# Performance work log

Measured on AMD Instinct MI355X. Metric: run time of the kernel, lower is better.

Reference implementation:

```python
import jax, jax.numpy as jnp
import numpy as np

LOG2PI = 1.837877  # exact constant used in source zeta()
K = 4              # pruning width (init arg k)


def _trans_child_multi(S00, S01, S11, tm0, tm1, g_mu, g_var):
    """Multiply 2D transition gaussian N([xc,xp]; t_mu, Sigma) with 1D child
    gaussian N(xc; g_mu, g_var), integrate out xc.
    Returns (log_scale, mu, var) of the resulting gaussian over the parent xp.
    Uses explicit 2x2 inverse/determinant exactly as the torch source does."""
    det_S = S00 * S11 - S01 * S01
    inv_det = 1.0 / det_S
    l00 = S11 * inv_det      # Lambda1 = Sigma^-1 (symmetric 2x2)
    l01 = -S01 * inv_det
    l11 = S00 * inv_det
    e1_0 = l00 * tm0 + l01 * tm1   # eta1 = Lambda1 @ t_mu
    e1_1 = l01 * tm0 + l11 * tm1
    # zeta1 = -0.5*(2*log2pi - log|Lambda1| + eta1^T Sigma eta1); log|Lambda1| = -log det_S
    q1 = e1_0 * (S00 * e1_0 + S01 * e1_1) + e1_1 * (S01 * e1_0 + S11 * e1_1)
    zeta1 = -0.5 * (2.0 * LOG2PI + jnp.log(det_S) + q1)
    lam2 = 1.0 / g_var
    zeta2 = -0.5 * (LOG2PI + jnp.log(g_var) + g_mu * g_mu * lam2)
    # Lambda_multi = Lambda1 + [[lam2,0],[0,0]]
    lm00 = l00 + lam2
    det_m = lm00 * l11 - l01 * l01
    inv_m = 1.0 / det_m
    vm00 = l11 * inv_m       # V_multi = Lambda_multi^-1
    vm01 = -l01 * inv_m
    vm11 = lm00 * inv_m
    em0 = e1_0 + g_mu * lam2  # eta_multi = eta1 + [eta2, 0]
    em1 = e1_1
    qm = em0 * (vm00 * em0 + vm01 * em1) + em1 * (vm01 * em0 + vm11 * em1)
    zetam = -0.5 * (2.0 * LOG2PI - jnp.log(det_m) + qm)
    scale = zeta1 + zeta2 - zetam
    mu = vm01 * em0 + vm11 * em1   # marginal over parent dim (second block)
    var = vm11
    return scale, mu, var


def _gauss1d_multi(m1, v1, m2, v2):
    """Product of two 1D gaussians -> (log_scale, mu, var)."""
    lam = 1.0 / v1 + 1.0 / v2
    vm = 1.0 / lam
    em = m1 / v1 + m2 / v2
    z1 = -0.5 * (LOG2PI + jnp.log(v1) + m1 * m1 / v1)
    z2 = -0.5 * (LOG2PI + jnp.log(v2) + m2 * m2 / v2)
    zm = -0.5 * (LOG2PI + jnp.log(vm) + em * em * vm)
    return z1 + z2 - zm, vm * em, vm


def setup_inputs():
    key = jax.random.key(0)
    k0, k1, k2, k3, k4, k5, k6 = jax.random.split(key, 7)
    B, L, V, NL = 64, 512, 150000, 46   # NL = num_labels(45) + 1 pad label
    tokens = jax.random.randint(k0, (B, L), 0, V)
    s_weight_table = 0.1 * jax.random.normal(k1, (V, NL), jnp.float32)
    s_mu_table = jax.random.normal(k2, (V, NL), jnp.float32)
    # var embeddings squared (A A^T for 1x1) in forward; keep away from 0
    s_var_table = 1.0 + 0.1 * jax.random.normal(k3, (V, NL), jnp.float32)
    t_weight = 0.1 * jax.random.normal(k4, (NL, NL), jnp.float32)
    t_mu = jax.random.normal(k5, (NL, NL, 2), jnp.float32)
    t_var_p = 1.0 + 0.1 * jax.random.normal(k6, (NL, NL, 3), jnp.float32)
    return {"tokens": tokens, "s_weight_table": s_weight_table,
            "s_mu_table": s_mu_table, "s_var_table": s_var_table,
            "t_weight": t_weight, "t_mu": t_mu, "t_var_p": t_var_p}


def _forward(tokens, s_weight_table, s_mu_table, s_var_table, t_weight, t_mu, t_var_p):
    B, L = tokens.shape
    NL = t_weight.shape[0]
    # state (emission) gaussian params via embedding lookups
    s_w = s_weight_table[tokens]            # [B,L,NL]
    s_m = s_mu_table[tokens]                # [B,L,NL]
    s_v = jnp.square(s_var_table[tokens])   # A A^T for the 1x1 case  [B,L,NL]
    # transition covariance: A = [[v0, v1], [0, v2]], Sigma = A A^T (as in source)
    v0, v1, v2 = t_var_p[..., 0], t_var_p[..., 1], t_var_p[..., 2]
    S00 = v0 * v0 + v1 * v1                 # [NL,NL]
    S01 = v1 * v2
    S11 = v2 * v2
    tm0, tm1 = t_mu[..., 0], t_mu[..., 1]
    NEG = jnp.float32(-1e30)

    def step(carry, xs):
        sc, mu, va = carry                  # inside mixture [B,K,NL] over child labels
        sw_t, sm_t, sv_t = xs               # emission at the next position [B,NL]
        scale2, mu2, var2 = _trans_child_multi(
            S00, S01, S11, tm0, tm1, mu[..., None], va[..., None])  # [B,K,C,P]
        scale2 = scale2 + sc[..., None] + t_weight
        # pruning: merge (component, child-label) dims, top-k per parent label
        def flat(x):
            return x.transpose(0, 3, 1, 2).reshape(B, NL, -1)   # [B,P,K*C]
        fs = flat(scale2)
        top_s, top_i = jax.lax.top_k(fs, K)                     # [B,P,K]
        top_m = jnp.take_along_axis(flat(mu2), top_i, axis=-1)
        top_v = jnp.take_along_axis(flat(var2), top_i, axis=-1)
        top_s = top_s.transpose(0, 2, 1)                        # [B,K,P]
        top_m = top_m.transpose(0, 2, 1)
        top_v = top_v.transpose(0, 2, 1)
        # multiply emission gaussian at the new position
        es, em, ev = _gauss1d_multi(top_m, top_v, sm_t[:, None, :], sv_t[:, None, :])
        new_sc = top_s + es + sw_t[:, None, :]
        return (new_sc, em, ev), None

    # init: emission at position 0 as the single real component, padded to K
    pad = jnp.full((B, K - 1, NL), NEG)
    sc0 = jnp.concatenate([s_w[:, 0][:, None], pad], axis=1)
    mu0 = jnp.concatenate([s_m[:, 0][:, None], jnp.zeros((B, K - 1, NL))], axis=1)
    va0 = jnp.concatenate([s_v[:, 0][:, None], jnp.ones((B, K - 1, NL))], axis=1)
    xs = (jnp.swapaxes(s_w[:, 1:], 0, 1),
          jnp.swapaxes(s_m[:, 1:], 0, 1),
          jnp.swapaxes(s_v[:, 1:], 0, 1))
    (sc, mu, va), _ = jax.lax.scan(step, (sc0, mu0, va0), xs)
    # each final gaussian integrates to exp(scale); inside score = logsumexp
    return jax.scipy.special.logsumexp(sc.reshape(B, -1), axis=-1)   # [B]


def reference(tokens, s_weight_table, s_mu_table, s_var_table, t_weight, t_mu, t_var_p):
    return _forward(tokens, s_weight_table, s_mu_table, s_var_table,
                    t_weight, t_mu, t_var_p)
```

## Files before the change

### kernel.cpp

```cpp
#include <hip/hip_runtime.h>

#define LOG2PI 1.837877f
#define LN2 0.6931471805599453f
#define RLN2 1.4426950408889634f
#define NLAB 46
#define KK 4
#define LSEQ 512
#define KC 184
#define BLOCK 832
#define NA 736
#define EMB 768

__device__ __forceinline__ float fastrcp(float x){ return __builtin_amdgcn_rcpf(x); }
__device__ __forceinline__ float flog2(float x){ return __builtin_amdgcn_logf(x); }
__device__ __forceinline__ float fmed3(float a, float b, float c){
    return __builtin_amdgcn_fmed3f(a, b, c);
}
template<int CTRL>
__device__ __forceinline__ float dppq(float v){
    return __uint_as_float((unsigned)__builtin_amdgcn_mov_dpp(
        (int)__float_as_uint(v), CTRL, 0xF, 0xF, false));
}
template<int OFF>
__device__ __forceinline__ float swz(float v){
    return __uint_as_float((unsigned)__builtin_amdgcn_ds_swizzle(
        (int)__float_as_uint(v), OFF));
}
template<int N> struct IC { static constexpr int value = N; };

__global__ __launch_bounds__(BLOCK, 4) void lveg_kernel(
    const int* __restrict__ tokens,
    const float* __restrict__ s_w_tab,
    const float* __restrict__ s_m_tab,
    const float* __restrict__ s_v_tab,
    const float* __restrict__ t_weight,
    const float* __restrict__ t_mu,
    const float* __restrict__ t_var_p,
    float* __restrict__ out)
{
    __shared__ float4 lam2v[2][NLAB];
    __shared__ float4 glamv[2][NLAB];
    __shared__ float4 z2sv[2][NLAB];
    __shared__ float  scv[KC];
    __shared__ float4 emi[2][NLAB];
    __shared__ int    tokL[LSEQ];
    __shared__ float4 tabA[NLAB*NLAB];
    __shared__ float2 tabB[NLAB*NLAB];

    const int b = blockIdx.x;
    const int tid = threadIdx.x;
    const int s = tid & 15;
    const int p = tid >> 4;
    const bool isA = (p < NLAB);
    const unsigned vmask2 = (s < 14) ? 0xFFFFFFFFu : 0u;
    const unsigned vorm2  = (s < 14) ? 0u : 0xFF800000u;
    const int c2 = (s < 14) ? (s + 32) : 0;
    const float NEGINF = __uint_as_float(0xFF800000u);

    for (int cp = tid; cp < NLAB*NLAB; cp += BLOCK) {
        float v0 = t_var_p[cp*3+0], v1 = t_var_p[cp*3+1], v2 = t_var_p[cp*3+2];
        float tm0 = t_mu[cp*2+0],  tm1 = t_mu[cp*2+1];
        float S00 = v0*v0 + v1*v1, S01 = v1*v2, S11 = v2*v2;
        float det = S00*S11 - S01*S01;
        float inv = 1.0f / det;
        float l00 = S11*inv, l01 = -S01*inv, l11 = S00*inv;
        float e0 = l00*tm0 + l01*tm1;
        float e1 = l01*tm0 + l11*tm1;
        float q1 = e0*(S00*e0 + S01*e1) + e1*(S01*e0 + S11*e1);
        float zeta1 = -0.5f*(2.0f*LOG2PI + __logf(det) + q1);
        tabA[cp] = make_float4(e0, e1, inv, l11);
        tabB[cp] = make_float2(l01, zeta1 + LOG2PI + t_weight[cp]);
    }
    for (int i = tid; i < LSEQ; i += BLOCK) tokL[i] = tokens[b*LSEQ + i];

    float rce0[3], rl11[3], rinv[3], rl11s[3], rqbs[3], rqes[3], rqcs[3], rAs[3];
    if (isA) {
#pragma unroll
        for (int ci = 0; ci < 3; ++ci) {
            int c = s + 16*ci;
            if (c < NLAB) {
                int cp = c*NLAB + p;
                float v0 = t_var_p[cp*3+0], v1 = t_var_p[cp*3+1], v2 = t_var_p[cp*3+2];
                float tm0 = t_mu[cp*2+0],  tm1 = t_mu[cp*2+1];
                float S00 = v0*v0 + v1*v1, S01 = v1*v2, S11 = v2*v2;
                float det = S00*S11 - S01*S01;
                float inv = 1.0f / det;
                float l00 = S11*inv, l01 = -S01*inv, l11 = S00*inv;
                float e0 = l00*tm0 + l01*tm1;
                float e1 = l01*tm0 + l11*tm1;
                float q1 = e0*(S00*e0 + S01*e1) + e1*(S01*e0 + S11*e1);
                float zeta1 = -0.5f*(2.0f*LOG2PI + __logf(det) + q1);
                rce0[ci]  = e0;
                rl11[ci]  = l11;
                rinv[ci]  = inv;
                rl11s[ci] = l11 * RLN2;
                rqbs[ci]  = 2.0f*l01*e1 * RLN2;
                rqes[ci]  = e1*e1 * RLN2;
                rqcs[ci]  = l00*e1*e1 * RLN2;
                rAs[ci]   = (zeta1 + LOG2PI + t_weight[cp]) * RLN2;
            } else {
                rce0[ci]=0.f; rl11[ci]=0.f; rinv[ci]=1.f; rl11s[ci]=0.f;
                rqbs[ci]=0.f; rqes[ci]=0.f; rqcs[ci]=0.f; rAs[ci]=0.f;
            }
        }
    }

    if (tid < NLAB) {
        int tok0 = tokens[b * LSEQ];
        float sw  = s_w_tab[tok0*NLAB + tid];
        float sm  = s_m_tab[tok0*NLAB + tid];
        float svr = s_v_tab[tok0*NLAB + tid];
        float gv = svr*svr;
        float lam2 = 1.0f / gv;
        float glam = sm * lam2;
        float z2 = -0.5f*(LOG2PI + __logf(gv) + sm*glam);
        float zpad = (-1e30f - 0.5f*LOG2PI) * RLN2;
        lam2v[0][tid] = make_float4(lam2, 1.0f, 1.0f, 1.0f);
        glamv[0][tid] = make_float4(glam, 0.0f, 0.0f, 0.0f);
        z2sv[0][tid]  = make_float4((sw + z2) * RLN2, zpad, zpad, zpad);
    }
    if (tid >= EMB) {
        int pe = tid - EMB;
        if (pe < NLAB) {
            int tok = tokens[b*LSEQ + 1];
            float sw  = s_w_tab[tok*NLAB + pe];
            float sm  = s_m_tab[tok*NLAB + pe];
            float svr = s_v_tab[tok*NLAB + pe];
            float sv = svr*svr;
            float rs = 1.0f / sv;
            float eb = sm * rs;
            float ez = -0.5f*(LOG2PI + __logf(sv) + sm*eb);
            emi[1][pe] = make_float4(sw, rs, eb, ez);
        }
    }
    __syncthreads();

    auto stepf = [&](auto CC, int t) {
        constexpr int CUR = decltype(CC)::value;
        if (isA) {
            float4 L0 = lam2v[CUR][s],      G0 = glamv[CUR][s],      Z0 = z2sv[CUR][s];
            float4 L1 = lam2v[CUR][s + 16], G1 = glamv[CUR][s + 16], Z1 = z2sv[CUR][s + 16];
            float4 L2 = lam2v[CUR][c2],     G2 = glamv[CUR][c2],     Z2 = z2sv[CUR][c2];
            __builtin_amdgcn_sched_barrier(0);
            float t0=NEGINF, t1=NEGINF, t2=NEGINF, t3=NEGINF;
#define CAND(ci, k, lam2, glam, z2s) {                                        \
            float em0 = rce0[ci] + (glam);                                    \
            float dm  = fmaf((lam2), rl11[ci], rinv[ci]);                     \
            float tA  = fmaf(rl11s[ci], em0, -rqbs[ci]);                      \
            float tB  = fmaf((lam2), rqes[ci], rqcs[ci]);                     \
            float Q   = fmaf(em0, tA, tB);                                    \
            float key = fmaf(0.5f, fmaf(Q, fastrcp(dm), -flog2(dm)),          \
                             rAs[ci] + (z2s));                                \
            unsigned kb = (__float_as_uint(key) & 0xFFFFFF00u)                \
                        | (unsigned)((k)*NLAB + s + 16*(ci));                 \
            if ((ci) == 2) kb = (kb & vmask2) | vorm2;                        \
            float fk = __uint_as_float(kb);                                   \
            float n0 = fmaxf(t0, fk);                                         \
            float n1 = fmed3(fk, t0, t1);                                     \
            float n2 = fmed3(fk, t1, t2);                                     \
            float n3 = fmed3(fk, t2, t3);                                     \
            t0=n0; t1=n1; t2=n2; t3=n3; }
            CAND(0, 0, L0.x, G0.x, Z0.x)  CAND(0, 1, L0.y, G0.y, Z0.y)
            CAND(0, 2, L0.z, G0.z, Z0.z)  CAND(0, 3, L0.w, G0.w, Z0.w)
            CAND(1, 0, L1.x, G1.x, Z1.x)  CAND(1, 1, L1.y, G1.y, Z1.y)
            CAND(1, 2, L1.z, G1.z, Z1.z)  CAND(1, 3, L1.w, G1.w, Z1.w)
            CAND(2, 0, L2.x, G2.x, Z2.x)  CAND(2, 1, L2.y, G2.y, Z2.y)
            CAND(2, 2, L2.z, G2.z, Z2.z)  CAND(2, 3, L2.w, G2.w, Z2.w)
#undef CAND
#define MSTAGE(F) { float b0=F(t0), b1=F(t1), b2=F(t2), b3=F(t3);                 \
                float M0=fmaxf(t0,b3), M1=fmaxf(t1,b2), M2=fmaxf(t2,b1), M3=fmaxf(t3,b0); \
                float x;                                                          \
                x=fmaxf(M0,M2); M2=fminf(M0,M2); M0=x;  x=fmaxf(M1,M3); M3=fminf(M1,M3); M1=x; \
                x=fmaxf(M0,M1); M1=fminf(M0,M1); M0=x;  x=fmaxf(M2,M3); M3=fminf(M2,M3); M2=x; \
                t0=M0; t1=M1; t2=M2; t3=M3; }
            MSTAGE(dppq<0xB1>)
            MSTAGE(dppq<0x4E>)
            MSTAGE(swz<0x101F>)
            {
                float b0=swz<0x201F>(t0), b1=swz<0x201F>(t1),
                      b2=swz<0x201F>(t2), b3=swz<0x201F>(t3);
                float M0=fmaxf(t0,b3), M1=fmaxf(t1,b2), M2=fmaxf(t2,b1), M3=fmaxf(t3,b0);
                t0=M0; t1=M1; t2=M2; t3=M3;
            }
#undef MSTAGE
            if (s < 4) {
                float sel = (s==0)?t0 : (s==1)?t1 : (s==2)?t2 : t3;
                unsigned kc = __float_as_uint(sel) & 0xFFu;
                unsigned k  = (kc * 1428u) >> 16;
                int c  = (int)kc - (int)k*NLAB;
                int cp = c*NLAB + p;
                float4 ta = tabA[cp];
                float2 tb = tabB[cp];
                float lam2 = ((const float*)&lam2v[CUR][0])[4*c + (int)k];
                float glam = ((const float*)&glamv[CUR][0])[4*c + (int)k];
                float z2s  = ((const float*)&z2sv[CUR][0])[4*c + (int)k] * LN2;
                float em0 = ta.x + glam;
                float em1 = ta.y;
                float l01 = tb.x;
                float l00 = fmaf(l01, l01, ta.z) * fastrcp(ta.w);
                float dm  = fmaf(lam2, ta.w, ta.z);
                float rdm = fastrcp(dm);
                float lm00 = l00 + lam2;
                float Q = fmaf(em0, fmaf(ta.w, em0, -2.0f*l01*em1), lm00*em1*em1);
                float score = fmaf(0.5f, fmaf(Q, rdm, -__logf(dm)), tb.y + z2s);
                float mu2  = rdm*(lm00*em1 - l01*em0);
                float var2 = lm00*rdm;
                float4 ev = emi[CUR ^ 1][p];
                float rv1 = fastrcp(var2);
                float lam = rv1 + ev.y;
                float emm = fmaf(mu2, rv1, ev.z);
                float vm  = fastrcp(lam);
                float z1 = -0.5f*(LOG2PI + __logf(var2) + mu2*mu2*rv1);
                float zm = -0.5f*(LOG2PI + __logf(vm) + emm*emm*vm);
                float nsc = score + (z1 + ev.w - zm) + ev.x;
                ((float*)&lam2v[CUR^1][p])[s] = lam;
                ((float*)&glamv[CUR^1][p])[s] = emm;
                ((float*)&z2sv[CUR^1][p])[s]  = (nsc + zm) * RLN2;
                scv[(int)s*NLAB + p] = nsc;
            }
        } else if (tid >= EMB) {
            int pe = tid - EMB;
            if (pe < NLAB && t + 1 < LSEQ) {
                int tok = tokL[t + 1];
                float sw  = s_w_tab[tok*NLAB + pe];
                float sm  = s_m_tab[tok*NLAB + pe];
                float svr = s_v_tab[tok*NLAB + pe];
                float sv = svr*svr;
                float rs = 1.0f / sv;
                float eb = sm * rs;
                float ez = -0.5f*(LOG2PI + __logf(sv) + sm*eb);
                emi[CUR][pe] = make_float4(sw, rs, eb, ez);
            }
        }
        __syncthreads();
    };

    int t = 1;
#pragma unroll 1
    for (int it = 0; it < (LSEQ - 2) / 2; ++it) {
        stepf(IC<0>{}, t); ++t;
        stepf(IC<1>{}, t); ++t;
    }
    stepf(IC<0>{}, t);

    if (tid < 64) {
        float mx = -1e38f;
        for (int i = tid; i < KC; i += 64) mx = fmaxf(mx, scv[i]);
#pragma unroll
        for (int m = 32; m; m >>= 1) mx = fmaxf(mx, __shfl_xor(mx, m, 64));
        float sum = 0.0f;
        for (int i = tid; i < KC; i += 64) sum += __expf(scv[i] - mx);
#pragma unroll
        for (int m = 32; m; m >>= 1) sum += __shfl_xor(sum, m, 64);
        if (tid == 0) out[b] = mx + __logf(sum);
    }
}

extern "C" void kernel_launch(void* const* d_in, const int* in_sizes, int n_in,
                              void* d_out, int out_size, void* d_ws, size_t ws_size,
                              hipStream_t stream) {
    const int*   tokens = (const int*)d_in[0];
    const float* sw     = (const float*)d_in[1];
    const float* sm     = (const float*)d_in[2];
    const float* sv     = (const float*)d_in[3];
    const float* tw     = (const float*)d_in[4];
    const float* tmu    = (const float*)d_in[5];
    const float* tvp    = (const float*)d_in[6];
    float* o = (float*)d_out;
    hipLaunchKernelGGL(lveg_kernel, dim3(64), dim3(BLOCK), 0, stream,
                       tokens, sw, sm, sv, tw, tmu, tvp, o);
}
```

Measured before the change: 1.182 ms.

## Pack per-component state into float2 pairs and vectorize candidate scoring

Replaces the three separate float4 shared arrays (lam2, glam, z2s) with one interleaved array of float2 pairs per label, grouped by pairs of pruned components. The candidate key computation is rewritten on 2-wide vectors so the compiler can emit packed FP32 operations (v_pk_fma/v_pk_mul) for two components at once. The goal is fewer VALU instructions in the hot per-step scoring loop. It adds strided index math for reads and writes, and the LDS load pattern changes from float4 to 64-bit loads, which may change bank behaviour.

```diff
diff --git a/kernel.cpp b/kernel.cpp
--- a/kernel.cpp
+++ b/kernel.cpp
@@ -11,6 +11,8 @@
 #define NA 736
 #define EMB 768
 
+typedef float v2f __attribute__((ext_vector_type(2)));
+
 __device__ __forceinline__ float fastrcp(float x){ return __builtin_amdgcn_rcpf(x); }
 __device__ __forceinline__ float flog2(float x){ return __builtin_amdgcn_logf(x); }
 __device__ __forceinline__ float fmed3(float a, float b, float c){
@@ -38,10 +40,8 @@
     const float* __restrict__ t_var_p,
     float* __restrict__ out)
 {
-    __shared__ float4 lam2v[2][NLAB];
-    __shared__ float4 glamv[2][NLAB];
-    __shared__ float4 z2sv[2][NLAB];
-    __shared__ float  scv[KC];
+    __shared__ v2f   pkc[2][NLAB][6];
+    __shared__ float scv[KC];
     __shared__ float4 emi[2][NLAB];
     __shared__ int    tokL[LSEQ];
     __shared__ float4 tabA[NLAB*NLAB];
@@ -115,9 +115,13 @@
         float glam = sm * lam2;
         float z2 = -0.5f*(LOG2PI + __logf(gv) + sm*glam);
         float zpad = (-1e30f - 0.5f*LOG2PI) * RLN2;
-        lam2v[0][tid] = make_float4(lam2, 1.0f, 1.0f, 1.0f);
-        glamv[0][tid] = make_float4(glam, 0.0f, 0.0f, 0.0f);
-        z2sv[0][tid]  = make_float4((sw + z2) * RLN2, zpad, zpad, zpad);
+        v2f r;
+        r.x = lam2; r.y = 1.0f;            pkc[0][tid][0] = r;
+        r.x = glam; r.y = 0.0f;            pkc[0][tid][1] = r;
+        r.x = (sw + z2)*RLN2; r.y = zpad;  pkc[0][tid][2] = r;
+        r.x = 1.0f; r.y = 1.0f;            pkc[0][tid][3] = r;
+        r.x = 0.0f; r.y = 0.0f;            pkc[0][tid][4] = r;
+        r.x = zpad; r.y = zpad;            pkc[0][tid][5] = r;
     }
     if (tid >= EMB) {
         int pe = tid - EMB;
@@ -138,21 +142,17 @@
     auto stepf = [&](auto CC, int t) {
         constexpr int CUR = decltype(CC)::value;
         if (isA) {
-            float4 L0 = lam2v[CUR][s],      G0 = glamv[CUR][s],      Z0 = z2sv[CUR][s];
-            float4 L1 = lam2v[CUR][s + 16], G1 = glamv[CUR][s + 16], Z1 = z2sv[CUR][s + 16];
-            float4 L2 = lam2v[CUR][c2],     G2 = glamv[CUR][c2],     Z2 = z2sv[CUR][c2];
+            const int cc[3] = {s, s + 16, c2};
+            v2f q[3][6];
+#pragma unroll
+            for (int ci = 0; ci < 3; ++ci)
+#pragma unroll
+                for (int j = 0; j < 6; ++j)
+                    q[ci][j] = pkc[CUR][cc[ci]][j];
             __builtin_amdgcn_sched_barrier(0);
             float t0=NEGINF, t1=NEGINF, t2=NEGINF, t3=NEGINF;
-#define CAND(ci, k, lam2, glam, z2s) {                                        \
-            float em0 = rce0[ci] + (glam);                                    \
-            float dm  = fmaf((lam2), rl11[ci], rinv[ci]);                     \
-            float tA  = fmaf(rl11s[ci], em0, -rqbs[ci]);                      \
-            float tB  = fmaf((lam2), rqes[ci], rqcs[ci]);                     \
-            float Q   = fmaf(em0, tA, tB);                                    \
-            float key = fmaf(0.5f, fmaf(Q, fastrcp(dm), -flog2(dm)),          \
-                             rAs[ci] + (z2s));                                \
-            unsigned kb = (__float_as_uint(key) & 0xFFFFFF00u)                \
-                        | (unsigned)((k)*NLAB + s + 16*(ci));                 \
+#define INS(kf, id, ci) {                                                     \
+            unsigned kb = (__float_as_uint(kf) & 0xFFFFFF00u) | (unsigned)(id); \
             if ((ci) == 2) kb = (kb & vmask2) | vorm2;                        \
             float fk = __uint_as_float(kb);                                   \
             float n0 = fmaxf(t0, fk);                                         \
@@ -160,13 +160,27 @@
             float n2 = fmed3(fk, t1, t2);                                     \
             float n3 = fmed3(fk, t2, t3);                                     \
             t0=n0; t1=n1; t2=n2; t3=n3; }
-            CAND(0, 0, L0.x, G0.x, Z0.x)  CAND(0, 1, L0.y, G0.y, Z0.y)
-            CAND(0, 2, L0.z, G0.z, Z0.z)  CAND(0, 3, L0.w, G0.w, Z0.w)
-            CAND(1, 0, L1.x, G1.x, Z1.x)  CAND(1, 1, L1.y, G1.y, Z1.y)
-            CAND(1, 2, L1.z, G1.z, Z1.z)  CAND(1, 3, L1.w, G1.w, Z1.w)
-            CAND(2, 0, L2.x, G2.x, Z2.x)  CAND(2, 1, L2.y, G2.y, Z2.y)
-            CAND(2, 2, L2.z, G2.z, Z2.z)  CAND(2, 3, L2.w, G2.w, Z2.w)
-#undef CAND
+#define CANDP(ci, pr) {                                                       \
+            v2f lamP  = q[ci][3*(pr)+0];                                      \
+            v2f glamP = q[ci][3*(pr)+1];                                      \
+            v2f zP    = q[ci][3*(pr)+2];                                      \
+            v2f em0 = glamP + rce0[ci];                                       \
+            v2f dm  = lamP * rl11[ci] + rinv[ci];                             \
+            v2f tA  = em0 * rl11s[ci] - rqbs[ci];                             \
+            v2f tB  = lamP * rqes[ci] + rqcs[ci];                             \
+            v2f Q   = em0 * tA + tB;                                          \
+            v2f rdm; rdm.x = fastrcp(dm.x); rdm.y = fastrcp(dm.y);            \
+            v2f lg;  lg.x  = flog2(dm.x);   lg.y  = flog2(dm.y);              \
+            v2f base  = zP + rAs[ci];                                         \
+            v2f inner = Q * rdm - lg;                                         \
+            v2f keyP  = 0.5f * inner + base;                                  \
+            INS(keyP.x, (2*(pr))*NLAB   + s + 16*(ci), ci)                    \
+            INS(keyP.y, (2*(pr)+1)*NLAB + s + 16*(ci), ci) }
+            CANDP(0, 0) CANDP(0, 1)
+            CANDP(1, 0) CANDP(1, 1)
+            CANDP(2, 0) CANDP(2, 1)
+#undef CANDP
+#undef INS
 #define MSTAGE(F) { float b0=F(t0), b1=F(t1), b2=F(t2), b3=F(t3);                 \
                 float M0=fmaxf(t0,b3), M1=fmaxf(t1,b2), M2=fmaxf(t2,b1), M3=fmaxf(t3,b0); \
                 float x;                                                          \
@@ -191,9 +205,11 @@
                 int cp = c*NLAB + p;
                 float4 ta = tabA[cp];
                 float2 tb = tabB[cp];
-                float lam2 = ((const float*)&lam2v[CUR][0])[4*c + (int)k];
-                float glam = ((const float*)&glamv[CUR][0])[4*c + (int)k];
-                float z2s  = ((const float*)&z2sv[CUR][0])[4*c + (int)k] * LN2;
+                const float* sp = (const float*)&pkc[CUR][c][0]
+                                  + 6*(int)(k >> 1) + (int)(k & 1);
+                float lam2 = sp[0];
+                float glam = sp[2];
+                float z2s  = sp[4] * LN2;
                 float em0 = ta.x + glam;
                 float em1 = ta.y;
                 float l01 = tb.x;
@@ -213,10 +229,11 @@
                 float z1 = -0.5f*(LOG2PI + __logf(var2) + mu2*mu2*rv1);
                 float zm = -0.5f*(LOG2PI + __logf(vm) + emm*emm*vm);
                 float nsc = score + (z1 + ev.w - zm) + ev.x;
-                ((float*)&lam2v[CUR^1][p])[s] = lam;
-                ((float*)&glamv[CUR^1][p])[s] = emm;
-                ((float*)&z2sv[CUR^1][p])[s]  = (nsc + zm) * RLN2;
-                scv[(int)s*NLAB + p] = nsc;
+                float* wp = (float*)&pkc[CUR ^ 1][p][0] + 6*(s >> 1) + (s & 1);
+                wp[0] = lam;
+                wp[2] = emm;
+                wp[4] = (nsc + zm) * RLN2;
+                scv[s*NLAB + p] = nsc;
             }
         } else if (tid >= EMB) {
             int pe = tid - EMB;
```

Result: faster. 1.138 ms (-3.8%).
